# Performance work log

Hardware: AMD Instinct MI355X
Metric: run time of the kernel (lower is better)

The kernel has to match this reference:

```python
import jax, jax.numpy as jnp
import numpy as np

B, T, D, K = 8, 2048, 384, 64

def setup_inputs() -> dict:
    key = jax.random.key(0)
    k1, k2, k3, k4 = jax.random.split(key, 4)
    x = jax.random.normal(k1, (B, T, D), dtype=jnp.float32)
    # torch nn.Linear default init scale ~ 1/sqrt(fan_in); use scaled normals
    Wq = jax.random.normal(k2, (D, K), dtype=jnp.float32) / np.sqrt(D)
    Wk = jax.random.normal(k3, (D, K), dtype=jnp.float32) / np.sqrt(D)
    Wv = jax.random.normal(k4, (D, D), dtype=jnp.float32) / np.sqrt(D)
    return {"x": x, "Wq": Wq, "Wk": Wk, "Wv": Wv}

def reference(x, Wq, Wk, Wv):
    # x: (B,T,D)
    q = jnp.einsum('btd,dk->btk', x, Wq)      # (B,T,K)
    k = jnp.einsum('btd,dk->btk', x, Wk)      # (B,T,K)
    v = jnp.einsum('btd,de->bte', x, Wv)      # (B,T,D)
    scores = jnp.einsum('bqk,bsk->bqs', q, k) / jnp.sqrt(jnp.float32(K))  # (B,T,T)
    causal = jnp.tril(jnp.ones((T, T), dtype=bool))
    scores = jnp.where(causal, scores, -jnp.inf)
    weights = jax.nn.softmax(scores, axis=-1)
    out = jnp.einsum('bqs,bse->bqe', weights, v)  # (B,T,D)
    return out
```

## Files before the change

kernel.cpp:

```cpp
#include <hip/hip_runtime.h>

#define TT 2048
#define DD 384

typedef float f32x4 __attribute__((ext_vector_type(4)));
typedef float f32x16 __attribute__((ext_vector_type(16)));
typedef short s16x8 __attribute__((ext_vector_type(8)));
typedef short s16x2 __attribute__((ext_vector_type(2)));
typedef unsigned int u32x4 __attribute__((ext_vector_type(4)));
typedef unsigned int u32x2 __attribute__((ext_vector_type(2)));

typedef __attribute__((address_space(3))) unsigned char* as3p;
typedef const __attribute__((address_space(1))) unsigned char* as1p;
#define GLLDS(gsrc, ldst) __builtin_amdgcn_global_load_lds((as1p)(gsrc), (as3p)(ldst), 16, 0, 0)

static __device__ __forceinline__ unsigned short f2bf(float f) {
    unsigned int u = __builtin_bit_cast(unsigned int, f);
    u = (u + 0x7fffu + ((u >> 16) & 1u)) >> 16;
    return (unsigned short)u;
}
static __device__ __forceinline__ unsigned int pk2(float a, float b) {
#if __has_builtin(__builtin_amdgcn_cvt_pk_bf16_f32)
    s16x2 t = __builtin_amdgcn_cvt_pk_bf16_f32(a, b);
    return __builtin_bit_cast(unsigned int, t);
#else
    unsigned int ua = __builtin_bit_cast(unsigned int, a);
    unsigned int ub = __builtin_bit_cast(unsigned int, b);
    ua = (ua + 0x7fffu + ((ua >> 16) & 1u)) >> 16;
    ub = (ub + 0x7fffu + ((ub >> 16) & 1u)) & 0xffff0000u;
    return ua | ub;
#endif
}

__global__ __launch_bounds__(256, 2) void qkv_gemm(
    const float* __restrict__ x, const float* __restrict__ Wq,
    const float* __restrict__ Wk, const float* __restrict__ Wv,
    unsigned short* __restrict__ qo, unsigned short* __restrict__ ko,
    unsigned short* __restrict__ vto)
{
    __shared__ __align__(16) unsigned short lds[16384];
    const int tid = threadIdx.x;
    const int l   = tid & 63;
    const int w   = tid >> 6;
    const int si  = l & 15;
    const int qq  = l >> 4;
    const int m0  = blockIdx.x * 128;
    const int nb  = blockIdx.y;
    const int wr  = w >> 1, wc = w & 1;

    const int bn = tid & 127;
    const int bk = (tid >> 7) * 16;
    const float* wsrc; int ldw;
    if (nb == 0) { wsrc = (bn < 64) ? (Wq + bn) : (Wk + (bn - 64)); ldw = 64; }
    else         { wsrc = Wv + (nb - 1) * 128 + bn;                 ldw = 384; }

    f32x4 acc[4][4];
    #pragma unroll
    for (int rt = 0; rt < 4; ++rt)
        #pragma unroll
        for (int ct = 0; ct < 4; ++ct) acc[rt][ct] = (f32x4){0.f, 0.f, 0.f, 0.f};

    for (int kt = 0; kt < 12; ++kt) {
        const int k0 = kt * 32;
        #pragma unroll
        for (int i = 0; i < 2; ++i) {
            const int u = tid + 256 * i, r = u >> 2, c = u & 3;
            const float* xp = x + (size_t)(m0 + r) * DD + k0 + c * 8;
            f32x4 x0 = *(const f32x4*)xp;
            f32x4 x1 = *(const f32x4*)(xp + 4);
            u32x4 av = (u32x4){pk2(x0[0], x0[1]), pk2(x0[2], x0[3]),
                               pk2(x1[0], x1[1]), pk2(x1[2], x1[3])};
            *(s16x8*)&lds[r * 32 + ((c ^ (r & 3)) * 8)] = __builtin_bit_cast(s16x8, av);
        }
        {
            float t[16];
            #pragma unroll
            for (int j = 0; j < 16; ++j) t[j] = wsrc[(size_t)(k0 + bk + j) * ldw];
            #pragma unroll
            for (int jj = 0; jj < 2; ++jj) {
                u32x4 bv = (u32x4){pk2(t[jj * 8 + 0], t[jj * 8 + 1]), pk2(t[jj * 8 + 2], t[jj * 8 + 3]),
                                   pk2(t[jj * 8 + 4], t[jj * 8 + 5]), pk2(t[jj * 8 + 6], t[jj * 8 + 7])};
                const int ch = (tid >> 7) * 2 + jj;
                *(s16x8*)&lds[4096 + bn * 32 + ((ch ^ (bn & 3)) * 8)] = __builtin_bit_cast(s16x8, bv);
            }
        }
        __syncthreads();

        s16x8 af[4], bf[4];
        #pragma unroll
        for (int rt = 0; rt < 4; ++rt) {
            const int row = wr * 64 + rt * 16 + si;
            af[rt] = *(const s16x8*)&lds[row * 32 + ((qq ^ (row & 3)) * 8)];
        }
        #pragma unroll
        for (int ct = 0; ct < 4; ++ct) {
            const int col = wc * 64 + ct * 16 + si;
            bf[ct] = *(const s16x8*)&lds[4096 + col * 32 + ((qq ^ (col & 3)) * 8)];
        }
        #pragma unroll
        for (int rt = 0; rt < 4; ++rt)
            #pragma unroll
            for (int ct = 0; ct < 4; ++ct)
                acc[rt][ct] = __builtin_amdgcn_mfma_f32_16x16x32_bf16(af[rt], bf[ct], acc[rt][ct], 0, 0, 0);
        __syncthreads();
    }

    if (nb == 0) {
        if (wc == 0) {
            #pragma unroll
            for (int rt = 0; rt < 4; ++rt)
                #pragma unroll
                for (int ct = 0; ct < 4; ++ct)
                    #pragma unroll
                    for (int r = 0; r < 4; ++r) {
                        const int m = m0 + wr * 64 + rt * 16 + qq * 4 + r;
                        qo[(size_t)m * 64 + ct * 16 + si] = f2bf(acc[rt][ct][r] * 0.125f);
                    }
        } else {
            #pragma unroll
            for (int rt = 0; rt < 4; ++rt)
                #pragma unroll
                for (int ct = 0; ct < 4; ++ct)
                    #pragma unroll
                    for (int r = 0; r < 4; ++r) {
                        const int m = m0 + wr * 64 + rt * 16 + qq * 4 + r;
                        const int col = ct * 16 + si;
                        ko[(size_t)m * 64 + (((col >> 3) ^ (m & 7)) * 8) + (col & 7)] = f2bf(acc[rt][ct][r]);
                    }
        }
    } else {
        #pragma unroll
        for (int rt = 0; rt < 4; ++rt)
            #pragma unroll
            for (int ct = 0; ct < 4; ++ct)
                #pragma unroll
                for (int r = 0; r < 4; ++r) {
                    const int m = wr * 64 + rt * 16 + qq * 4 + r;
                    const int n = wc * 64 + ct * 16 + si;
                    lds[n * 128 + (((m >> 3) ^ (n & 7)) * 8) + (m & 7)] = f2bf(acc[rt][ct][r]);
                }
        __syncthreads();
        const int bbat = m0 >> 11, t0 = m0 & 2047;
        #pragma unroll
        for (int i = 0; i < 8; ++i) {
            const int u = tid + 256 * i, n = u >> 4, mc = u & 15;
            s16x8 v = *(const s16x8*)&lds[n * 128 + ((mc ^ (n & 7)) * 8)];
            *(s16x8*)&vto[((size_t)bbat * DD + ((nb - 1) * 128 + n)) * TT
                          + t0 + (mc >> 3) * 64 + (((mc & 7) ^ (n & 7)) * 8)] = v;
        }
    }
}

__global__ __launch_bounds__(256, 2) void attn(
    const unsigned short* __restrict__ qg, const unsigned short* __restrict__ kg,
    const unsigned short* __restrict__ vg, float* __restrict__ out)
{
    __shared__ __align__(16) unsigned short lds[40960];

    const int tid = threadIdx.x;
    const int l   = tid & 63;
    const int w   = tid >> 6;
    const int qh  = w >> 1;
    const int eg  = w & 1;
    const int lo  = l & 31;
    const int hi  = l >> 5;

    const int g    = blockIdx.x;
    const int bb   = g & 7;
    const int rest = g >> 3;
    const int eh   = rest % 3;
    const int q2   = 31 - rest / 3;
    const int q0   = q2 * 64;
    const int e0   = eh * 128;
    const int qrow = q0 + qh * 32 + lo;

    s16x8 qf[4];
    {
        const unsigned short* qp = qg + ((size_t)bb * TT + qrow) * 64;
        #pragma unroll
        for (int st = 0; st < 4; ++st) qf[st] = *(const s16x8*)(qp + st * 16 + hi * 8);
    }

    f32x16 o[2];
    #pragma unroll
    for (int et = 0; et < 2; ++et)
        #pragma unroll
        for (int r = 0; r < 16; ++r) o[et][r] = 0.f;
    float lp = 0.f;

    const unsigned short* kbase = kg + (size_t)bb * TT * 64;
    const unsigned short* vbase = vg + ((size_t)bb * DD + e0) * TT;

    #define STAGE(IT, KB, VB)                                                              \
    {                                                                                      \
        GLLDS(kbase + (size_t)(IT) * 4096 + (2 * w) * 512 + l * 8,                         \
              &lds[(KB) * 4096 + (2 * w) * 512]);                                          \
        GLLDS(kbase + (size_t)(IT) * 4096 + (2 * w + 1) * 512 + l * 8,                     \
              &lds[(KB) * 4096 + (2 * w + 1) * 512]);                                      \
        _Pragma("unroll")                                                                  \
        for (int c3 = 0; c3 < 4; ++c3) {                                                   \
            const int rg = 4 * w + c3;                                                     \
            GLLDS(vbase + (size_t)(rg * 8 + (l >> 3)) * TT + (IT) * 64 + (l & 7) * 8,      \
                  &lds[8192 + (VB) * 8192 + rg * 512]);                                    \
        }                                                                                  \
    }

    #define PVSTEP(VB, PB)                                                                 \
    {                                                                                      \
        __builtin_amdgcn_s_setprio(1);                                                     \
        _Pragma("unroll")                                                                  \
        for (int ss = 0; ss < 2; ++ss) {                                                   \
            s16x8 a0 = *(const s16x8*)&lds[32768 + (PB) * 4096 + (qh * 2 + ss) * 1024 + l * 8];       \
            s16x8 a1 = *(const s16x8*)&lds[32768 + (PB) * 4096 + (qh * 2 + ss) * 1024 + 512 + l * 8]; \
            _Pragma("unroll")                                                              \
            for (int et = 0; et < 2; ++et) {                                               \
                const int el = eg * 64 + et * 32 + lo;                                     \
                const int vbse = 8192 + (VB) * 8192 + el * 64;                             \
                s16x8 v0 = *(const s16x8*)&lds[vbse + (((ss * 4 + hi) ^ (el & 7)) * 8)];   \
                o[et] = __builtin_amdgcn_mfma_f32_32x32x16_bf16(a0, v0, o[et], 0, 0, 0);   \
                s16x8 v1 = *(const s16x8*)&lds[vbse + (((ss * 4 + 2 + hi) ^ (el & 7)) * 8)]; \
                o[et] = __builtin_amdgcn_mfma_f32_32x32x16_bf16(a1, v1, o[et], 0, 0, 0);   \
            }                                                                              \
        }                                                                                  \
        __builtin_amdgcn_s_setprio(0);                                                     \
    }

    STAGE(0, 0, 0);

    int vi = 0, vn = 1;
    for (int it = 0; it <= q2; ++it) {
        const int kb = it & 1;
        __syncthreads();

        if (it < q2) STAGE(it + 1, 1 - kb, vn);

        {
            f32x16 sa;
            #pragma unroll
            for (int r = 0; r < 16; ++r) sa[r] = 0.f;
            __builtin_amdgcn_s_setprio(1);
            #pragma unroll
            for (int st = 0; st < 4; ++st) {
                s16x8 kf = *(const s16x8*)&lds[kb * 4096 + (eg * 32 + lo) * 64 + (((st * 2 + hi) ^ (lo & 7)) * 8)];
                sa = __builtin_amdgcn_mfma_f32_32x32x16_bf16(kf, qf[st], sa, 0, 0, 0);
            }
            __builtin_amdgcn_s_setprio(0);
            const bool mb = (it == q2);
            float pv[16];
            #pragma unroll
            for (int r = 0; r < 16; ++r) {
                float e = __expf(sa[r]);
                if (mb) {
                    const int srow = it * 64 + eg * 32 + (r & 3) + 8 * (r >> 2) + 4 * hi;
                    if (srow > qrow) e = 0.f;
                }
                pv[r] = e;
                lp += e;
            }
            unsigned int d0 = pk2(pv[0], pv[1]),   d1 = pk2(pv[2], pv[3]);
            unsigned int d2 = pk2(pv[4], pv[5]),   d3 = pk2(pv[6], pv[7]);
            unsigned int d4 = pk2(pv[8], pv[9]),   d5 = pk2(pv[10], pv[11]);
            unsigned int d6 = pk2(pv[12], pv[13]), d7 = pk2(pv[14], pv[15]);
            u32x4 fa0, fa1;
#if __has_builtin(__builtin_amdgcn_permlane32_swap)
            {
                u32x2 s02 = __builtin_bit_cast(u32x2, __builtin_amdgcn_permlane32_swap(d0, d2, false, false));
                u32x2 s13 = __builtin_bit_cast(u32x2, __builtin_amdgcn_permlane32_swap(d1, d3, false, false));
                u32x2 s46 = __builtin_bit_cast(u32x2, __builtin_amdgcn_permlane32_swap(d4, d6, false, false));
                u32x2 s57 = __builtin_bit_cast(u32x2, __builtin_amdgcn_permlane32_swap(d5, d7, false, false));
                fa0 = (u32x4){s02[0], s13[0], s02[1], s13[1]};
                fa1 = (u32x4){s46[0], s57[0], s46[1], s57[1]};
            }
#else
            {
                unsigned int sA0 = hi ? d0 : d2, sA1 = hi ? d1 : d3;
                unsigned int rA0 = (unsigned int)__shfl_xor((int)sA0, 32);
                unsigned int rA1 = (unsigned int)__shfl_xor((int)sA1, 32);
                fa0 = hi ? (u32x4){rA0, rA1, d2, d3} : (u32x4){d0, d1, rA0, rA1};
                unsigned int sB0 = hi ? d4 : d6, sB1 = hi ? d5 : d7;
                unsigned int rB0 = (unsigned int)__shfl_xor((int)sB0, 32);
                unsigned int rB1 = (unsigned int)__shfl_xor((int)sB1, 32);
                fa1 = hi ? (u32x4){rB0, rB1, d6, d7} : (u32x4){d4, d5, rB0, rB1};
            }
#endif
            *(s16x8*)&lds[32768 + kb * 4096 + (qh * 2 + eg) * 1024 + l * 8]       = __builtin_bit_cast(s16x8, fa0);
            *(s16x8*)&lds[32768 + kb * 4096 + (qh * 2 + eg) * 1024 + 512 + l * 8] = __builtin_bit_cast(s16x8, fa1);
        }

        if (it > 0) {
            const int vp = (vi == 0) ? 2 : vi - 1;
            PVSTEP(vp, 1 - kb);
        }

        vi = vn; vn = (vn == 2) ? 0 : vn + 1;
    }
    __syncthreads();
    {
        const int vlast = (vi == 0) ? 2 : vi - 1;
        PVSTEP(vlast, q2 & 1);
    }
    __syncthreads();

    float* stL = (float*)&lds[32768];
    lp += __shfl_xor(lp, 32);
    if (hi == 0) stL[(qh * 2 + eg) * 32 + lo] = lp;
    __syncthreads();

    #pragma unroll
    for (int et = 0; et < 2; ++et)
        #pragma unroll
        for (int r = 0; r < 16; ++r) {
            const int rloc = (r & 3) + 8 * (r >> 2) + 4 * hi;
            const float linv = 1.f / (stL[qh * 64 + rloc] + stL[qh * 64 + 32 + rloc]);
            out[((size_t)bb * TT + q0 + qh * 32 + rloc) * DD + e0 + eg * 64 + et * 32 + lo]
                = o[et][r] * linv;
        }
    #undef STAGE
    #undef PVSTEP
}

extern "C" void kernel_launch(void* const* d_in, const int* in_sizes, int n_in,
                              void* d_out, int out_size, void* d_ws, size_t ws_size,
                              hipStream_t stream)
{
    const float* x  = (const float*)d_in[0];
    const float* Wq = (const float*)d_in[1];
    const float* Wk = (const float*)d_in[2];
    const float* Wv = (const float*)d_in[3];

    unsigned short* qws  = (unsigned short*)d_ws;
    unsigned short* kws  = (unsigned short*)((char*)d_ws + ((size_t)2 << 20));
    unsigned short* vtws = (unsigned short*)((char*)d_ws + ((size_t)4 << 20));

    qkv_gemm<<<dim3(128, 4), dim3(256), 0, stream>>>(x, Wq, Wk, Wv, qws, kws, vtws);
    attn<<<dim3(768), dim3(256), 0, stream>>>(qws, kws, vtws, (float*)d_out);
}
```

Measured before the change: 138.7 us.

## Restructure attention into 12-wave blocks with paired causal tiles and wider E

The attention kernel now launches 256 blocks of 768 threads. Each block handles half of the output columns (192) and processes two query tiles, a long one and a short one (31-pr and pr), so causal work is balanced across blocks. Four waves compute QK^T and softmax while all twelve waves do PV over 32 columns each. The K and V loads are split between the score waves and the other waves. This cuts redundant QK^T recomputation, since each tile's scores are now computed twice instead of three times, and it evens out the load. In exchange it adds a large block, barriers between phases, and waves that sit idle during the softmax.

```diff
diff --git a/kernel.cpp b/kernel.cpp
--- a/kernel.cpp
+++ b/kernel.cpp
@@ -151,57 +151,44 @@
     }
 }
 
-__global__ __launch_bounds__(256, 2) void attn(
+__global__ __launch_bounds__(768, 3) void attn(
     const unsigned short* __restrict__ qg, const unsigned short* __restrict__ kg,
     const unsigned short* __restrict__ vg, float* __restrict__ out)
 {
-    __shared__ __align__(16) unsigned short lds[40960];
+    __shared__ __align__(16) unsigned short lds[53248];
 
     const int tid = threadIdx.x;
     const int l   = tid & 63;
     const int w   = tid >> 6;
-    const int qh  = w >> 1;
-    const int eg  = w & 1;
+    const int qh  = w & 1;
+    const int eu  = w >> 1;
+    const bool isprod = (w < 4);
     const int lo  = l & 31;
     const int hi  = l >> 5;
 
-    const int g    = blockIdx.x;
-    const int bb   = g & 7;
-    const int rest = g >> 3;
-    const int eh   = rest % 3;
-    const int q2   = 31 - rest / 3;
-    const int q0   = q2 * 64;
-    const int e0   = eh * 128;
-    const int qrow = q0 + qh * 32 + lo;
-
-    s16x8 qf[4];
-    {
-        const unsigned short* qp = qg + ((size_t)bb * TT + qrow) * 64;
-        #pragma unroll
-        for (int st = 0; st < 4; ++st) qf[st] = *(const s16x8*)(qp + st * 16 + hi * 8);
-    }
-
-    f32x16 o[2];
-    #pragma unroll
-    for (int et = 0; et < 2; ++et)
-        #pragma unroll
-        for (int r = 0; r < 16; ++r) o[et][r] = 0.f;
-    float lp = 0.f;
+    const int g  = blockIdx.x;
+    const int bb = g & 7;
+    const int eh = (g >> 3) & 1;
+    const int pr = g >> 4;
+    const int e0 = eh * 192;
 
     const unsigned short* kbase = kg + (size_t)bb * TT * 64;
     const unsigned short* vbase = vg + ((size_t)bb * DD + e0) * TT;
 
     #define STAGE(IT, KB, VB)                                                              \
     {                                                                                      \
-        GLLDS(kbase + (size_t)(IT) * 4096 + (2 * w) * 512 + l * 8,                         \
-              &lds[(KB) * 4096 + (2 * w) * 512]);                                          \
-        GLLDS(kbase + (size_t)(IT) * 4096 + (2 * w + 1) * 512 + l * 8,                     \
-              &lds[(KB) * 4096 + (2 * w + 1) * 512]);                                      \
-        _Pragma("unroll")                                                                  \
-        for (int c3 = 0; c3 < 4; ++c3) {                                                   \
-            const int rg = 4 * w + c3;                                                     \
-            GLLDS(vbase + (size_t)(rg * 8 + (l >> 3)) * TT + (IT) * 64 + (l & 7) * 8,      \
-                  &lds[8192 + (VB) * 8192 + rg * 512]);                                    \
+        if (isprod) {                                                                      \
+            GLLDS(kbase + (size_t)(IT) * 4096 + (2 * w) * 512 + l * 8,                     \
+                  &lds[(KB) * 4096 + (2 * w) * 512]);                                      \
+            GLLDS(kbase + (size_t)(IT) * 4096 + (2 * w + 1) * 512 + l * 8,                 \
+                  &lds[(KB) * 4096 + (2 * w + 1) * 512]);                                  \
+        } else {                                                                           \
+            _Pragma("unroll")                                                              \
+            for (int c3 = 0; c3 < 3; ++c3) {                                               \
+                const int rg = 3 * (w - 4) + c3;                                           \
+                GLLDS(vbase + (size_t)(rg * 8 + (l >> 3)) * TT + (IT) * 64 + (l & 7) * 8,  \
+                      &lds[8192 + (VB) * 12288 + rg * 512]);                               \
+            }                                                                              \
         }                                                                                  \
     }
 
@@ -210,111 +197,128 @@
         __builtin_amdgcn_s_setprio(1);                                                     \
         _Pragma("unroll")                                                                  \
         for (int ss = 0; ss < 2; ++ss) {                                                   \
-            s16x8 a0 = *(const s16x8*)&lds[32768 + (PB) * 4096 + (qh * 2 + ss) * 1024 + l * 8];       \
-            s16x8 a1 = *(const s16x8*)&lds[32768 + (PB) * 4096 + (qh * 2 + ss) * 1024 + 512 + l * 8]; \
-            _Pragma("unroll")                                                              \
-            for (int et = 0; et < 2; ++et) {                                               \
-                const int el = eg * 64 + et * 32 + lo;                                     \
-                const int vbse = 8192 + (VB) * 8192 + el * 64;                             \
-                s16x8 v0 = *(const s16x8*)&lds[vbse + (((ss * 4 + hi) ^ (el & 7)) * 8)];   \
-                o[et] = __builtin_amdgcn_mfma_f32_32x32x16_bf16(a0, v0, o[et], 0, 0, 0);   \
-                s16x8 v1 = *(const s16x8*)&lds[vbse + (((ss * 4 + 2 + hi) ^ (el & 7)) * 8)]; \
-                o[et] = __builtin_amdgcn_mfma_f32_32x32x16_bf16(a1, v1, o[et], 0, 0, 0);   \
-            }                                                                              \
+            const int pbse = 45056 + (PB) * 4096 + (qh * 2 + ss) * 1024;                   \
+            s16x8 a0 = *(const s16x8*)&lds[pbse + l * 8];                                  \
+            s16x8 a1 = *(const s16x8*)&lds[pbse + 512 + l * 8];                            \
+            const int el = eu * 32 + lo;                                                   \
+            const int vbse = 8192 + (VB) * 12288 + el * 64;                                \
+            s16x8 v0 = *(const s16x8*)&lds[vbse + (((ss * 4 + hi) ^ (el & 7)) * 8)];       \
+            o = __builtin_amdgcn_mfma_f32_32x32x16_bf16(a0, v0, o, 0, 0, 0);               \
+            s16x8 v1 = *(const s16x8*)&lds[vbse + (((ss * 4 + 2 + hi) ^ (el & 7)) * 8)];   \
+            o = __builtin_amdgcn_mfma_f32_32x32x16_bf16(a1, v1, o, 0, 0, 0);               \
         }                                                                                  \
         __builtin_amdgcn_s_setprio(0);                                                     \
     }
 
-    STAGE(0, 0, 0);
-
-    int vi = 0, vn = 1;
-    for (int it = 0; it <= q2; ++it) {
-        const int kb = it & 1;
-        __syncthreads();
-
-        if (it < q2) STAGE(it + 1, 1 - kb, vn);
-
+    for (int hf = 0; hf < 2; ++hf) {
+        const int q2 = hf ? pr : 31 - pr;
+        const int q0 = q2 * 64;
+        const int qrow = q0 + qh * 32 + lo;
+
+        s16x8 qf[4];
+        if (isprod) {
+            const unsigned short* qp = qg + ((size_t)bb * TT + qrow) * 64;
+            #pragma unroll
+            for (int st = 0; st < 4; ++st) qf[st] = *(const s16x8*)(qp + st * 16 + hi * 8);
+        }
+
+        f32x16 o;
+        #pragma unroll
+        for (int r = 0; r < 16; ++r) o[r] = 0.f;
+        float lp = 0.f;
+
+        STAGE(0, 0, 0);
+
+        int vi = 0, vn = 1;
+        for (int it = 0; it <= q2; ++it) {
+            const int kb = it & 1;
+            __syncthreads();
+
+            if (it < q2) STAGE(it + 1, 1 - kb, vn);
+
+            if (isprod) {
+                f32x16 sa;
+                #pragma unroll
+                for (int r = 0; r < 16; ++r) sa[r] = 0.f;
+                __builtin_amdgcn_s_setprio(1);
+                #pragma unroll
+                for (int st = 0; st < 4; ++st) {
+                    s16x8 kf = *(const s16x8*)&lds[kb * 4096 + (eu * 32 + lo) * 64 + (((st * 2 + hi) ^ (lo & 7)) * 8)];
+                    sa = __builtin_amdgcn_mfma_f32_32x32x16_bf16(kf, qf[st], sa, 0, 0, 0);
+                }
+                __builtin_amdgcn_s_setprio(0);
+                const bool mb = (it == q2);
+                float pv[16];
+                #pragma unroll
+                for (int r = 0; r < 16; ++r) {
+                    float e = __expf(sa[r]);
+                    if (mb) {
+                        const int srow = it * 64 + eu * 32 + (r & 3) + 8 * (r >> 2) + 4 * hi;
+                        if (srow > qrow) e = 0.f;
+                    }
+                    pv[r] = e;
+                    lp += e;
+                }
+                unsigned int d0 = pk2(pv[0], pv[1]),   d1 = pk2(pv[2], pv[3]);
+                unsigned int d2 = pk2(pv[4], pv[5]),   d3 = pk2(pv[6], pv[7]);
+                unsigned int d4 = pk2(pv[8], pv[9]),   d5 = pk2(pv[10], pv[11]);
+                unsigned int d6 = pk2(pv[12], pv[13]), d7 = pk2(pv[14], pv[15]);
+                u32x4 fa0, fa1;
+#if __has_builtin(__builtin_amdgcn_permlane32_swap)
+                {
+                    u32x2 s02 = __builtin_bit_cast(u32x2, __builtin_amdgcn_permlane32_swap(d0, d2, false, false));
+                    u32x2 s13 = __builtin_bit_cast(u32x2, __builtin_amdgcn_permlane32_swap(d1, d3, false, false));
+                    u32x2 s46 = __builtin_bit_cast(u32x2, __builtin_amdgcn_permlane32_swap(d4, d6, false, false));
+                    u32x2 s57 = __builtin_bit_cast(u32x2, __builtin_amdgcn_permlane32_swap(d5, d7, false, false));
+                    fa0 = (u32x4){s02[0], s13[0], s02[1], s13[1]};
+                    fa1 = (u32x4){s46[0], s57[0], s46[1], s57[1]};
+                }
+#else
+                {
+                    unsigned int sA0 = hi ? d0 : d2, sA1 = hi ? d1 : d3;
+                    unsigned int rA0 = (unsigned int)__shfl_xor((int)sA0, 32);
+                    unsigned int rA1 = (unsigned int)__shfl_xor((int)sA1, 32);
+                    fa0 = hi ? (u32x4){rA0, rA1, d2, d3} : (u32x4){d0, d1, rA0, rA1};
+                    unsigned int sB0 = hi ? d4 : d6, sB1 = hi ? d5 : d7;
+                    unsigned int rB0 = (unsigned int)__shfl_xor((int)sB0, 32);
+                    unsigned int rB1 = (unsigned int)__shfl_xor((int)sB1, 32);
+                    fa1 = hi ? (u32x4){rB0, rB1, d6, d7} : (u32x4){d4, d5, rB0, rB1};
+                }
+#endif
+                *(s16x8*)&lds[45056 + kb * 4096 + (qh * 2 + eu) * 1024 + l * 8]       = __builtin_bit_cast(s16x8, fa0);
+                *(s16x8*)&lds[45056 + kb * 4096 + (qh * 2 + eu) * 1024 + 512 + l * 8] = __builtin_bit_cast(s16x8, fa1);
+            }
+
+            if (it > 0) {
+                const int vp = (vi == 0) ? 2 : vi - 1;
+                PVSTEP(vp, 1 - kb);
+            }
+
+            vi = vn; vn = (vn == 2) ? 0 : vn + 1;
+        }
+        __syncthreads();
         {
-            f32x16 sa;
-            #pragma unroll
-            for (int r = 0; r < 16; ++r) sa[r] = 0.f;
-            __builtin_amdgcn_s_setprio(1);
-            #pragma unroll
-            for (int st = 0; st < 4; ++st) {
-                s16x8 kf = *(const s16x8*)&lds[kb * 4096 + (eg * 32 + lo) * 64 + (((st * 2 + hi) ^ (lo & 7)) * 8)];
-                sa = __builtin_amdgcn_mfma_f32_32x32x16_bf16(kf, qf[st], sa, 0, 0, 0);
+            const int vlast = (vi == 0) ? 2 : vi - 1;
+            PVSTEP(vlast, q2 & 1);
+        }
+        if (isprod) {
+            float lt = lp + __shfl_xor(lp, 32);
+            if (hi == 0) ((float*)lds)[(qh * 2 + eu) * 32 + lo] = lt;
+        }
+        __syncthreads();
+
+        {
+            const float* stL = (const float*)lds;
+            #pragma unroll
+            for (int r = 0; r < 16; ++r) {
+                const int rloc = (r & 3) + 8 * (r >> 2) + 4 * hi;
+                const float linv = 1.f / (stL[(qh * 2) * 32 + rloc] + stL[(qh * 2 + 1) * 32 + rloc]);
+                out[((size_t)bb * TT + q0 + qh * 32 + rloc) * DD + e0 + eu * 32 + lo]
+                    = o[r] * linv;
             }
-            __builtin_amdgcn_s_setprio(0);
-            const bool mb = (it == q2);
-            float pv[16];
-            #pragma unroll
-            for (int r = 0; r < 16; ++r) {
-                float e = __expf(sa[r]);
-                if (mb) {
-                    const int srow = it * 64 + eg * 32 + (r & 3) + 8 * (r >> 2) + 4 * hi;
-                    if (srow > qrow) e = 0.f;
-                }
-                pv[r] = e;
-                lp += e;
-            }
-            unsigned int d0 = pk2(pv[0], pv[1]),   d1 = pk2(pv[2], pv[3]);
-            unsigned int d2 = pk2(pv[4], pv[5]),   d3 = pk2(pv[6], pv[7]);
-            unsigned int d4 = pk2(pv[8], pv[9]),   d5 = pk2(pv[10], pv[11]);
-            unsigned int d6 = pk2(pv[12], pv[13]), d7 = pk2(pv[14], pv[15]);
-            u32x4 fa0, fa1;
-#if __has_builtin(__builtin_amdgcn_permlane32_swap)
-            {
-                u32x2 s02 = __builtin_bit_cast(u32x2, __builtin_amdgcn_permlane32_swap(d0, d2, false, false));
-                u32x2 s13 = __builtin_bit_cast(u32x2, __builtin_amdgcn_permlane32_swap(d1, d3, false, false));
-                u32x2 s46 = __builtin_bit_cast(u32x2, __builtin_amdgcn_permlane32_swap(d4, d6, false, false));
-                u32x2 s57 = __builtin_bit_cast(u32x2, __builtin_amdgcn_permlane32_swap(d5, d7, false, false));
-                fa0 = (u32x4){s02[0], s13[0], s02[1], s13[1]};
-                fa1 = (u32x4){s46[0], s57[0], s46[1], s57[1]};
-            }
-#else
-            {
-                unsigned int sA0 = hi ? d0 : d2, sA1 = hi ? d1 : d3;
-                unsigned int rA0 = (unsigned int)__shfl_xor((int)sA0, 32);
-                unsigned int rA1 = (unsigned int)__shfl_xor((int)sA1, 32);
-                fa0 = hi ? (u32x4){rA0, rA1, d2, d3} : (u32x4){d0, d1, rA0, rA1};
-                unsigned int sB0 = hi ? d4 : d6, sB1 = hi ? d5 : d7;
-                unsigned int rB0 = (unsigned int)__shfl_xor((int)sB0, 32);
-                unsigned int rB1 = (unsigned int)__shfl_xor((int)sB1, 32);
-                fa1 = hi ? (u32x4){rB0, rB1, d6, d7} : (u32x4){d4, d5, rB0, rB1};
-            }
-#endif
-            *(s16x8*)&lds[32768 + kb * 4096 + (qh * 2 + eg) * 1024 + l * 8]       = __builtin_bit_cast(s16x8, fa0);
-            *(s16x8*)&lds[32768 + kb * 4096 + (qh * 2 + eg) * 1024 + 512 + l * 8] = __builtin_bit_cast(s16x8, fa1);
-        }
-
-        if (it > 0) {
-            const int vp = (vi == 0) ? 2 : vi - 1;
-            PVSTEP(vp, 1 - kb);
-        }
-
-        vi = vn; vn = (vn == 2) ? 0 : vn + 1;
-    }
-    __syncthreads();
-    {
-        const int vlast = (vi == 0) ? 2 : vi - 1;
-        PVSTEP(vlast, q2 & 1);
-    }
-    __syncthreads();
-
-    float* stL = (float*)&lds[32768];
-    lp += __shfl_xor(lp, 32);
-    if (hi == 0) stL[(qh * 2 + eg) * 32 + lo] = lp;
-    __syncthreads();
-
-    #pragma unroll
-    for (int et = 0; et < 2; ++et)
-        #pragma unroll
-        for (int r = 0; r < 16; ++r) {
-            const int rloc = (r & 3) + 8 * (r >> 2) + 4 * hi;
-            const float linv = 1.f / (stL[qh * 64 + rloc] + stL[qh * 64 + 32 + rloc]);
-            out[((size_t)bb * TT + q0 + qh * 32 + rloc) * DD + e0 + eg * 64 + et * 32 + lo]
-                = o[et][r] * linv;
-        }
+        }
+        __syncthreads();
+    }
     #undef STAGE
     #undef PVSTEP
 }
@@ -333,5 +337,5 @@
     unsigned short* vtws = (unsigned short*)((char*)d_ws + ((size_t)4 << 20));
 
     qkv_gemm<<<dim3(128, 4), dim3(256), 0, stream>>>(x, Wq, Wk, Wv, qws, kws, vtws);
-    attn<<<dim3(768), dim3(256), 0, stream>>>(qws, kws, vtws, (float*)d_out);
-}
+    attn<<<dim3(256), dim3(768), 0, stream>>>(qws, kws, vtws, (float*)d_out);
+}
```

Measured after the change: 133.4 us. 3.9% less time.
